# Kernel optimization log

Measured on AMD Instinct MI355X. Metric: run time of the kernel, lower is better.

## Reference

```python
import jax, jax.numpy as jnp
import numpy as np

N = 50000      # nodes
E = 800000     # edges (before self-loops)
F_IN = 128     # input node features
H = 5          # attention heads
C = 32         # per-head channels (hidden_channels // 5)
HC = H * C     # 160 = hidden_channels
G = 64         # graphs in batch


def setup_inputs() -> dict:
    key = jax.random.key(0)
    ks = jax.random.split(key, 20)
    p = lambda k, shape: jax.random.normal(k, shape, dtype=jnp.float32) * 0.1
    return {
        "x": jax.random.normal(ks[0], (N, F_IN), dtype=jnp.float32),
        "edge_index": jax.random.randint(ks[1], (2, E), 0, N),
        "edge_attr": jax.random.normal(ks[2], (E, 1), dtype=jnp.float32),
        "batch": jnp.sort(jax.random.randint(ks[3], (N,), 0, G)),
        # conv1 params (GATConv: lin, lin_edge, att_src, att_dst, att_edge, bias)
        "w1": p(ks[4], (F_IN, HC)), "we1": p(ks[5], (1, HC)),
        "as1": p(ks[6], (H, C)), "ad1": p(ks[7], (H, C)), "ae1": p(ks[8], (H, C)),
        "b1": jnp.zeros((HC,), jnp.float32),
        # conv2 params
        "w2": p(ks[9], (HC, HC)), "we2": p(ks[10], (1, HC)),
        "as2": p(ks[11], (H, C)), "ad2": p(ks[12], (H, C)), "ae2": p(ks[13], (H, C)),
        "b2": jnp.zeros((HC,), jnp.float32),
        # LayerNorms + merge MLP
        "ln1_g": jnp.ones((HC,), jnp.float32), "ln1_b": jnp.zeros((HC,), jnp.float32),
        "ln2_g": jnp.ones((HC,), jnp.float32), "ln2_b": jnp.zeros((HC,), jnp.float32),
        "mw": p(ks[14], (HC, HC)), "mb": jnp.zeros((HC,), jnp.float32),
    }


def _layernorm(x, g, b, eps=1e-5):
    m = x.mean(-1, keepdims=True)
    v = ((x - m) ** 2).mean(-1, keepdims=True)
    return (x - m) / jnp.sqrt(v + eps) * g + b


def _gat_layer(x, edge_index, edge_attr, w, we, a_s, a_d, a_e, b):
    """PyG GATConv with edge_dim, add_self_loops=True, fill_value='mean'."""
    src, dst = edge_index[0], edge_index[1]
    # self-loop edge_attr = mean of incoming edge attrs (scatter-mean onto dst)
    cnt = jax.ops.segment_sum(jnp.ones((E,), x.dtype), dst, num_segments=N)
    ea_mean = jax.ops.segment_sum(edge_attr, dst, num_segments=N) / jnp.maximum(cnt, 1.0)[:, None]
    loop = jnp.arange(N)
    src_f = jnp.concatenate([src, loop])
    dst_f = jnp.concatenate([dst, loop])
    ea_f = jnp.concatenate([edge_attr, ea_mean], axis=0)  # [E+N, 1]

    h = (x @ w).reshape(N, H, C)                           # [N,H,C]
    al_src = jnp.einsum('nhc,hc->nh', h, a_s)              # [N,H]
    al_dst = jnp.einsum('nhc,hc->nh', h, a_d)
    eh = (ea_f @ we).reshape(-1, H, C)                     # [E+N,H,C]
    al_e = jnp.einsum('ehc,hc->eh', eh, a_e)

    alpha = jax.nn.leaky_relu(al_src[src_f] + al_dst[dst_f] + al_e, 0.2)  # [E+N,H]
    amax = jax.ops.segment_max(alpha, dst_f, num_segments=N)
    ex = jnp.exp(alpha - amax[dst_f])
    den = jax.ops.segment_sum(ex, dst_f, num_segments=N)
    alpha = ex / den[dst_f]                                # segment softmax over dst

    out = jax.ops.segment_sum(h[src_f] * alpha[..., None], dst_f, num_segments=N)
    return out.reshape(N, HC) + b, alpha


def reference(x, edge_index, edge_attr, batch,
              w1, we1, as1, ad1, ae1, b1,
              w2, we2, as2, ad2, ae2, b2,
              ln1_g, ln1_b, ln2_g, ln2_b, mw, mb):
    x1, a1 = _gat_layer(x, edge_index, edge_attr, w1, we1, as1, ad1, ae1, b1)
    x1 = jax.nn.leaky_relu(x1, 0.01)
    x1 = _layernorm(x1, ln1_g, ln1_b)          # dropout = identity in eval
    x2, a2 = _gat_layer(x1, edge_index, edge_attr, w2, we2, as2, ad2, ae2, b2)
    x2 = jax.nn.leaky_relu(x2, 0.01)
    x2 = _layernorm(x2, ln2_g, ln2_b)
    x3 = jax.nn.leaky_relu(x2 @ mw + mb, 0.01)
    gcnt = jax.ops.segment_sum(jnp.ones((N,), x3.dtype), batch, num_segments=G)
    pooled = jax.ops.segment_sum(x3, batch, num_segments=G) / jnp.maximum(gcnt, 1.0)[:, None]
    return x3, pooled, a1, a2
```

## Files before the change

### kernel.cpp

```cpp
#include <hip/hip_runtime.h>
#include <hip/hip_fp16.h>
#include <math.h>

#define NN 50000
#define EE 800000
#define FIN 128
#define NH 5
#define HC 160
#define NG 64
#define CH2 32
#define NB 160
#define EPB 5000
#define NW 12500
#define ALS8 8
#define LOG2E 1.4426950408889634f
#define WPAD 168
#define IPAD 40

typedef _Float16 f16x8 __attribute__((ext_vector_type(8)));
typedef _Float16 f16x4 __attribute__((ext_vector_type(4)));
typedef float f32x4 __attribute__((ext_vector_type(4)));

__device__ __forceinline__ float lrelu(float x, float s) { return x >= 0.f ? x : s * x; }

__device__ __forceinline__ float4 h8_to_f4(uint2 u) {
    __half2 a = *reinterpret_cast<__half2*>(&u.x);
    __half2 b = *reinterpret_cast<__half2*>(&u.y);
    float2 fa = __half22float2(a), fb = __half22float2(b);
    return make_float4(fa.x, fa.y, fb.x, fb.y);
}

__global__ void prep_kernel(const int* __restrict__ batch, float* psum, int* gcnt,
                            const float* we1, const float* ae1,
                            const float* we2, const float* ae2, float* s_out,
                            int* dbin) {
    int i = blockIdx.x * 256 + threadIdx.x;
    if (i < NG * HC) psum[i] = 0.f;
    if (i < 256) dbin[i] = 0;
    if (i < NG) {
        int lo = 0, hi = NN;
        while (lo < hi) { int m = (lo + hi) >> 1; if (batch[m] < i) lo = m + 1; else hi = m; }
        int s = lo;
        lo = 0; hi = NN;
        int g1 = i + 1;
        while (lo < hi) { int m = (lo + hi) >> 1; if (batch[m] < g1) lo = m + 1; else hi = m; }
        gcnt[i] = lo - s;
    }
    if (i < 10) {
        const float* we = (i < 5) ? we1 : we2;
        const float* ae = (i < 5) ? ae1 : ae2;
        int h = i % 5;
        float s = 0.f;
        for (int c = 0; c < 32; c++) s += we[h * 32 + c] * ae[h * 32 + c];
        s_out[i] = s * LOG2E;
    }
}

__global__ void prepw_kernel(const float* __restrict__ w1, const float* __restrict__ w2,
                             const float* __restrict__ mw,
                             __half* wt1, __half* wt2, __half* wt3) {
    int i = blockIdx.x * 256 + threadIdx.x;
    if (i < 160 * 128) {
        int c = i >> 7, k = i & 127;
        wt1[i] = __float2half(w1[k * HC + c]);
    }
    if (i < 160 * 160) {
        int c = i / 160, k = i - c * 160;
        wt2[i] = __float2half(w2[k * HC + c]);
        wt3[i] = __float2half(mw[k * HC + c]);
    }
}

__global__ __launch_bounds__(256) void hist_kernel(const int* __restrict__ ei,
                                                   unsigned* __restrict__ hist_g) {
    __shared__ unsigned lh[NW];
    int b = blockIdx.x, tid = threadIdx.x;
    for (int w = tid; w < NW; w += 256) lh[w] = 0;
    __syncthreads();
    const int* dstp = ei + EE + b * EPB;
    for (int i = tid; i < EPB; i += 256) {
        int d = dstp[i];
        atomicAdd(&lh[d >> 2], 1u << ((d & 3) * 8));
    }
    __syncthreads();
    unsigned* outp = hist_g + (size_t)b * NW;
    for (int w = tid; w < NW; w += 256) outp[w] = lh[w];
}

__global__ void sscan_kernel(const unsigned* __restrict__ hist_g,
                             unsigned short* __restrict__ base_g, int* __restrict__ deg,
                             int* __restrict__ dbin) {
    __shared__ int lbin[256];
    int tid = threadIdx.x;
    int w = blockIdx.x * 256 + tid;
    lbin[tid] = 0;
    __syncthreads();
    if (w < NW) {
        unsigned r0 = 0, r1 = 0, r2 = 0, r3 = 0;
        for (int b = 0; b < NB; b++) {
            unsigned x = hist_g[(size_t)b * NW + w];
            uint2 st;
            st.x = r0 | (r1 << 16);
            st.y = r2 | (r3 << 16);
            *reinterpret_cast<uint2*>(&base_g[(size_t)b * NN + 4 * w]) = st;
            r0 += x & 0xffu; r1 += (x >> 8) & 0xffu; r2 += (x >> 16) & 0xffu; r3 += (x >> 24) & 0xffu;
        }
        uint4 dv; dv.x = r0; dv.y = r1; dv.z = r2; dv.w = r3;
        *reinterpret_cast<uint4*>(&deg[4 * w]) = dv;
        atomicAdd(&lbin[255 - (int)(r0 > 255u ? 255u : r0)], 1);
        atomicAdd(&lbin[255 - (int)(r1 > 255u ? 255u : r1)], 1);
        atomicAdd(&lbin[255 - (int)(r2 > 255u ? 255u : r2)], 1);
        atomicAdd(&lbin[255 - (int)(r3 > 255u ? 255u : r3)], 1);
    }
    __syncthreads();
    if (lbin[tid]) atomicAdd(&dbin[tid], lbin[tid]);
}

__global__ void scan1_kernel(const int* __restrict__ deg, int* bsum) {
    __shared__ int ws[4];
    int tid = threadIdx.x, lane = tid & 63, wid = tid >> 6;
    int i = blockIdx.x * 256 + tid;
    int v = (i < NN) ? deg[i] : 0;
    for (int o = 32; o >= 1; o >>= 1) v += __shfl_down(v, o, 64);
    if (lane == 0) ws[wid] = v;
    __syncthreads();
    if (tid == 0) bsum[blockIdx.x] = ws[0] + ws[1] + ws[2] + ws[3];
}

__global__ void scan2_kernel(int* bsum, int* boff, const int* __restrict__ dbin,
                             int* __restrict__ dpos) {
    __shared__ int ws[4];
    int tid = threadIdx.x, lane = tid & 63, wid = tid >> 6;
    int v = (tid < 196) ? bsum[tid] : 0;
    int x = v;
    for (int o = 1; o < 64; o <<= 1) {
        int t = __shfl_up(x, o, 64);
        if (lane >= o) x += t;
    }
    if (lane == 63) ws[wid] = x;
    __syncthreads();
    if (tid == 0) {
        int acc = 0;
        for (int w = 0; w < 4; w++) { int t = ws[w]; ws[w] = acc; acc += t; }
    }
    __syncthreads();
    if (tid < 196) boff[tid] = x + ws[wid] - v;
    __syncthreads();
    int bv = dbin[tid];
    int bx = bv;
    for (int o = 1; o < 64; o <<= 1) {
        int t = __shfl_up(bx, o, 64);
        if (lane >= o) bx += t;
    }
    if (lane == 63) ws[wid] = bx;
    __syncthreads();
    if (tid == 0) {
        int acc = 0;
        for (int w = 0; w < 4; w++) { int t = ws[w]; ws[w] = acc; acc += t; }
    }
    __syncthreads();
    dpos[tid] = bx + ws[wid] - bv;
}

__global__ void scan3_kernel(const int* __restrict__ deg, const int* __restrict__ boff,
                             int* off, int* __restrict__ dpos, int* __restrict__ perm) {
    __shared__ int ws[4];
    __shared__ int lbin[256];
    __shared__ int lbase[256];
    int tid = threadIdx.x, lane = tid & 63, wid = tid >> 6;
    int i = blockIdx.x * 256 + tid;
    int v = (i < NN) ? deg[i] : 0;
    lbin[tid] = 0;
    int x = v;
    for (int o = 1; o < 64; o <<= 1) {
        int t = __shfl_up(x, o, 64);
        if (lane >= o) x += t;
    }
    if (lane == 63) ws[wid] = x;
    __syncthreads();
    if (tid == 0) {
        int acc = 0;
        for (int w = 0; w < 4; w++) { int t = ws[w]; ws[w] = acc; acc += t; }
    }
    __syncthreads();
    int incl = x + ws[wid] + boff[blockIdx.x];
    int bin = 255 - (v > 255 ? 255 : v);
    int rank = 0;
    if (i < NN) {
        off[i + 1] = incl;
        rank = atomicAdd(&lbin[bin], 1);
    }
    if (i == 0) off[0] = 0;
    __syncthreads();
    if (lbin[tid] > 0) lbase[tid] = atomicAdd(&dpos[tid], lbin[tid]);
    __syncthreads();
    if (i < NN) perm[lbase[bin] + rank] = i;
}

__global__ __launch_bounds__(256) void scatter_kernel(const int* __restrict__ ei,
                                                      const float* __restrict__ ea,
                                                      const unsigned short* __restrict__ base_g,
                                                      const int* __restrict__ soff,
                                                      uint4* __restrict__ erec) {
    __shared__ unsigned lc[NW];
    int b = blockIdx.x, tid = threadIdx.x;
    for (int w = tid; w < NW; w += 256) lc[w] = 0;
    __syncthreads();
    int e0 = b * EPB;
    const unsigned short* brow = base_g + (size_t)b * NN;
    for (int i = tid; i < EPB; i += 256) {
        int e = e0 + i;
        int d = ei[EE + e];
        int sh = (d & 3) * 8;
        unsigned old = atomicAdd(&lc[d >> 2], 1u << sh);
        int r = (int)((old >> sh) & 0xffu);
        int pos = soff[d] + (int)brow[d] + r;
        uint4 rec;
        rec.x = (unsigned)ei[e];
        rec.y = (unsigned)e;
        rec.z = __float_as_uint(ea[e]);
        rec.w = 0;
        erec[pos] = rec;
    }
}

template <int K, typename AT>
__global__ __launch_bounds__(128, 4) void gemm_kernel(const AT* __restrict__ A,
                                                      const __half* __restrict__ Wt,
                                                      const float* __restrict__ a_s,
                                                      const float* __restrict__ a_d,
                                                      __half* __restrict__ out,
                                                      float* __restrict__ al_s,
                                                      float* __restrict__ al_d) {
    __shared__ __align__(16) char smem[16640];
    _Float16* Alds = (_Float16*)smem;
    _Float16* Bt   = (_Float16*)(smem + 2560);
    _Float16* Clds = (_Float16*)(smem + 2560);
    float* asld = (float*)(smem + 15360);
    float* adld = (float*)(smem + 16000);
    const int tid = threadIdx.x;
    const int w = tid >> 6, l = tid & 63;
    const int lr = l & 15, lq = l >> 4;
    const int base = blockIdx.x * 32;

    for (int i = tid; i < 160; i += 128) { asld[i] = a_s[i]; adld[i] = a_d[i]; }

    f32x4 acc[2][5];
#pragma unroll
    for (int mt = 0; mt < 2; mt++)
#pragma unroll
        for (int t = 0; t < 5; t++) acc[mt][t] = (f32x4){0.f, 0.f, 0.f, 0.f};

    for (int k0 = 0; k0 < K; k0 += 32) {
        __syncthreads();
        if constexpr (sizeof(AT) == 4) {
            for (int f = tid; f < 256; f += 128) {
                int row = f >> 3, q = f & 7;
                float4 av = make_float4(0.f, 0.f, 0.f, 0.f);
                if (base + row < NN)
                    av = *reinterpret_cast<const float4*>(&A[(size_t)(base + row) * K + k0 + q * 4]);
                f16x4 hv = {(_Float16)av.x, (_Float16)av.y, (_Float16)av.z, (_Float16)av.w};
                *reinterpret_cast<f16x4*>(&Alds[row * 40 + q * 4]) = hv;
            }
        } else {
            int row = tid >> 2, q = tid & 3;
            uint4 v = make_uint4(0, 0, 0, 0);
            if (base + row < NN)
                v = *reinterpret_cast<const uint4*>(&A[(size_t)(base + row) * K + k0 + q * 8]);
            *reinterpret_cast<uint4*>(&Alds[row * 40 + q * 8]) = v;
        }
        for (int f = tid; f < 640; f += 128) {
            int c = f >> 2, q = f & 3;
            uint4 v = *reinterpret_cast<const uint4*>(&Wt[(size_t)c * K + k0 + q * 8]);
            *reinterpret_cast<uint4*>(&Bt[c * 40 + q * 8]) = v;
        }
        __syncthreads();
        const f16x8 a0 = *reinterpret_cast<const f16x8*>(&Alds[lr * 40 + lq * 8]);
        const f16x8 a1 = *reinterpret_cast<const f16x8*>(&Alds[(16 + lr) * 40 + lq * 8]);
#pragma unroll
        for (int t = 0; t < 5; t++) {
            const f16x8 b = *reinterpret_cast<const f16x8*>(
                &Bt[((w * 5 + t) * 16 + lr) * 40 + lq * 8]);
            acc[0][t] = __builtin_amdgcn_mfma_f32_16x16x32_f16(a0, b, acc[0][t], 0, 0, 0);
            acc[1][t] = __builtin_amdgcn_mfma_f32_16x16x32_f16(a1, b, acc[1][t], 0, 0, 0);
        }
    }
    __syncthreads();
    _Float16* Cw = Clds + w * (32 * 88);
#pragma unroll
    for (int mt = 0; mt < 2; mt++)
#pragma unroll
        for (int t = 0; t < 5; t++)
#pragma unroll
            for (int j = 0; j < 4; j++)
                Cw[(mt * 16 + lq * 4 + j) * 88 + t * 16 + lr] = (_Float16)acc[mt][t][j];
    __syncthreads();
    for (int i = l; i < 320; i += 64) {
        int row = i / 10, q = i - row * 10;
        if (base + row < NN) {
            uint4 v = *reinterpret_cast<const uint4*>(&Cw[row * 88 + q * 8]);
            *reinterpret_cast<uint4*>(&out[(size_t)(base + row) * HC + w * 80 + q * 8]) = v;
        }
    }
    for (int f = tid; f < 320; f += 128) {
        int row = f / 10, rem = f - row * 10;
        int h = rem >> 1, sd = rem & 1;
        if (base + row < NN) {
            const float* av = (sd ? adld : asld) + h * 32;
            float s = 0.f;
#pragma unroll
            for (int c = 0; c < 32; c++) {
                int col = h * 32 + c;
                int wv = col >= 80;
                s += (float)Clds[wv * (32 * 88) + row * 88 + (col - 80 * wv)] * av[c];
            }
            s *= LOG2E;
            if (sd) al_d[(size_t)(base + row) * NH + h] = s;
            else    al_s[(size_t)(base + row) * ALS8 + h] = s;
        }
    }
}

__global__ __launch_bounds__(256, 8) void aggregate_kernel(
    const int* __restrict__ perm,
    const int* __restrict__ soff, const uint4* __restrict__ erec,
    const __half* __restrict__ hfeat, const float* __restrict__ als,
    const float* __restrict__ al_d, const float* __restrict__ s_e,
    const float* __restrict__ bias, const float* __restrict__ g_ln,
    const float* __restrict__ b_ln,
    float* __restrict__ alpha_out, __half* __restrict__ x_out) {
    const int tid = threadIdx.x;
    const int grp = tid >> 4;
    const int sl = tid & 15;
    const int n = perm[blockIdx.x * 16 + grp];
    __shared__ float w_sh_all[16][WPAD];
    __shared__ int ioff_all[16][IPAD];
    float* w_sh = w_sh_all[grp];
    int* ioff_sh = ioff_all[grp];

    const int s0 = soff[n];
    const int deg = soff[n + 1] - s0;
    const int items = deg + 1;

    float adr[NH], ser[NH];
#pragma unroll
    for (int h = 0; h < NH; h++) { adr[h] = al_d[n * NH + h]; ser[h] = s_e[h]; }

    const int cA = sl * 4, cB = 64 + sl * 4, cC = 128 + sl * 2;
    const int hA = sl >> 3, hB = 2 + (sl >> 3);
    float4 accA = make_float4(0.f, 0.f, 0.f, 0.f);
    float4 accB = make_float4(0.f, 0.f, 0.f, 0.f);
    float2 accC = make_float2(0.f, 0.f);

    if (items <= CH2) {
        float rw[2][NH];
        float lm[NH];
#pragma unroll
        for (int h = 0; h < NH; h++) lm[h] = -3.0e38f;
        float eas = 0.f;
        int myy[2];
#pragma unroll
        for (int t = 0; t < 2; t++) {
            if (deg > 16 * t) {
                int i = sl + 16 * t;
                if (i < deg) {
                    uint4 rec = erec[s0 + i];
                    int src = (int)rec.x;
                    float eav = __uint_as_float(rec.z);
                    ioff_sh[i] = src * (HC * 2);
                    myy[t] = (int)rec.y;
                    eas += eav;
                    const float* ap = als + (size_t)src * ALS8;
                    float4 a4 = *reinterpret_cast<const float4*>(ap);
                    float a5 = ap[4];
                    float asv[5] = {a4.x, a4.y, a4.z, a4.w, a5};
#pragma unroll
                    for (int h = 0; h < NH; h++) {
                        float r = lrelu(asv[h] + adr[h] + eav * ser[h], 0.2f);
                        rw[t][h] = r;
                        lm[h] = fmaxf(lm[h], r);
                    }
                }
            }
        }
#pragma unroll
        for (int o = 1; o < 16; o <<= 1) {
#pragma unroll
            for (int h = 0; h < NH; h++) lm[h] = fmaxf(lm[h], __shfl_xor(lm[h], o, 64));
            eas += __shfl_xor(eas, o, 64);
        }
        float emean = eas / fmaxf((float)deg, 1.f);
        float m[NH], rs[NH];
        {
            const float* ap = als + (size_t)n * ALS8;
            float4 a4 = *reinterpret_cast<const float4*>(ap);
            float a5 = ap[4];
            float asv[5] = {a4.x, a4.y, a4.z, a4.w, a5};
#pragma unroll
            for (int h = 0; h < NH; h++) {
                rs[h] = lrelu(asv[h] + adr[h] + emean * ser[h], 0.2f);
                m[h] = fmaxf(lm[h], rs[h]);
            }
        }
        float ls[NH] = {0.f, 0.f, 0.f, 0.f, 0.f};
#pragma unroll
        for (int t = 0; t < 2; t++) {
            if (items > 16 * t) {
                int i = sl + 16 * t;
                if (i < deg) {
#pragma unroll
                    for (int h = 0; h < NH; h++) {
                        float w = exp2f(rw[t][h] - m[h]);
                        rw[t][h] = w;
                        ls[h] += w;
                    }
                } else if (i == deg) {
                    ioff_sh[i] = n * (HC * 2);
#pragma unroll
                    for (int h = 0; h < NH; h++) {
                        float w = exp2f(rs[h] - m[h]);
                        rw[t][h] = w;
                        ls[h] += w;
                    }
                }
            }
        }
#pragma unroll
        for (int o = 1; o < 16; o <<= 1) {
#pragma unroll
            for (int h = 0; h < NH; h++) ls[h] += __shfl_xor(ls[h], o, 64);
        }
        float dinv[NH];
#pragma unroll
        for (int h = 0; h < NH; h++) dinv[h] = 1.f / ls[h];
#pragma unroll
        for (int t = 0; t < 2; t++) {
            if (items > 16 * t) {
                int i = sl + 16 * t;
                if (i < items) {
                    int opos = (i < deg) ? myy[t] : (EE + n);
#pragma unroll
                    for (int h = 0; h < NH; h++) {
                        float w = rw[t][h] * dinv[h];
                        w_sh[i * NH + h] = w;
                        alpha_out[(size_t)opos * NH + h] = w;
                    }
                }
            }
        }
        const char* hb = (const char*)hfeat;
        for (int i0 = 0; i0 < items; i0 += 4) {
            float wA[4], wB[4], wC[4];
            uint2 vA[4], vB[4];
            unsigned vC[4];
#pragma unroll
            for (int j = 0; j < 4; j++) {
                int i = i0 + j;
                bool ok = i < items;
                int ii = ok ? i : 0;
                const char* rp = hb + (size_t)(unsigned)ioff_sh[ii];
                wA[j] = ok ? w_sh[ii * NH + hA] : 0.f;
                wB[j] = ok ? w_sh[ii * NH + hB] : 0.f;
                wC[j] = ok ? w_sh[ii * NH + 4] : 0.f;
                vA[j] = *reinterpret_cast<const uint2*>(rp + cA * 2);
                vB[j] = *reinterpret_cast<const uint2*>(rp + cB * 2);
                vC[j] = *reinterpret_cast<const unsigned*>(rp + cC * 2);
            }
#pragma unroll
            for (int j = 0; j < 4; j++) {
                float4 fA = h8_to_f4(vA[j]);
                accA.x += wA[j] * fA.x; accA.y += wA[j] * fA.y;
                accA.z += wA[j] * fA.z; accA.w += wA[j] * fA.w;
                float4 fB = h8_to_f4(vB[j]);
                accB.x += wB[j] * fB.x; accB.y += wB[j] * fB.y;
                accB.z += wB[j] * fB.z; accB.w += wB[j] * fB.w;
                __half2 pC = *reinterpret_cast<__half2*>(&vC[j]);
                accC.x += wC[j] * __low2float(pC);
                accC.y += wC[j] * __high2float(pC);
            }
        }
    } else {
        float lm[NH];
#pragma unroll
        for (int h = 0; h < NH; h++) lm[h] = -3.0e38f;
        float eas = 0.f;
        for (int i = sl; i < deg; i += 16) {
            uint4 rec = erec[s0 + i];
            int src = (int)rec.x;
            float eav = __uint_as_float(rec.z);
            eas += eav;
            const float* ap = als + (size_t)src * ALS8;
            float4 a4 = *reinterpret_cast<const float4*>(ap);
            float a5 = ap[4];
            float asv[5] = {a4.x, a4.y, a4.z, a4.w, a5};
#pragma unroll
            for (int h = 0; h < NH; h++) {
                float r = lrelu(asv[h] + adr[h] + eav * ser[h], 0.2f);
                lm[h] = fmaxf(lm[h], r);
            }
        }
#pragma unroll
        for (int o = 1; o < 16; o <<= 1) {
#pragma unroll
            for (int h = 0; h < NH; h++) lm[h] = fmaxf(lm[h], __shfl_xor(lm[h], o, 64));
            eas += __shfl_xor(eas, o, 64);
        }
        float emean = eas / fmaxf((float)deg, 1.f);
        float m[NH], rs[NH];
        {
            const float* ap = als + (size_t)n * ALS8;
#pragma unroll
            for (int h = 0; h < NH; h++) {
                rs[h] = lrelu(ap[h] + adr[h] + emean * ser[h], 0.2f);
                m[h] = fmaxf(lm[h], rs[h]);
            }
        }
        float ls[NH] = {0.f, 0.f, 0.f, 0.f, 0.f};
        for (int i = sl; i < items; i += 16) {
            int src; float eav;
            if (i < deg) { uint4 rec = erec[s0 + i]; src = (int)rec.x; eav = __uint_as_float(rec.z); }
            else         { src = n; eav = emean; }
            const float* ap = als + (size_t)src * ALS8;
#pragma unroll
            for (int h = 0; h < NH; h++) {
                float r = lrelu(ap[h] + adr[h] + eav * ser[h], 0.2f);
                ls[h] += exp2f(r - m[h]);
            }
        }
#pragma unroll
        for (int o = 1; o < 16; o <<= 1) {
#pragma unroll
            for (int h = 0; h < NH; h++) ls[h] += __shfl_xor(ls[h], o, 64);
        }
        float dinv[NH];
#pragma unroll
        for (int h = 0; h < NH; h++) dinv[h] = 1.f / ls[h];
        for (int i = sl; i < items; i += 16) {
            int src; float eav; int opos;
            if (i < deg) { uint4 rec = erec[s0 + i]; src = (int)rec.x; eav = __uint_as_float(rec.z); opos = (int)rec.y; }
            else         { src = n; eav = emean; opos = EE + n; }
            const float* ap = als + (size_t)src * ALS8;
#pragma unroll
            for (int h = 0; h < NH; h++) {
                float r = lrelu(ap[h] + adr[h] + eav * ser[h], 0.2f);
                alpha_out[(size_t)opos * NH + h] = exp2f(r - m[h]) * dinv[h];
            }
        }
        for (int i = 0; i < items; i++) {
            int src; float eav;
            if (i < deg) { uint4 rec = erec[s0 + i]; src = (int)rec.x; eav = __uint_as_float(rec.z); }
            else         { src = n; eav = emean; }
            const float* ap = als + (size_t)src * ALS8;
            float wAv = exp2f(lrelu(ap[hA] + adr[hA] + eav * ser[hA], 0.2f) - m[hA]) * dinv[hA];
            float wBv = exp2f(lrelu(ap[hB] + adr[hB] + eav * ser[hB], 0.2f) - m[hB]) * dinv[hB];
            float wCv = exp2f(lrelu(ap[4] + adr[4] + eav * ser[4], 0.2f) - m[4]) * dinv[4];
            const char* rp = (const char*)hfeat + (size_t)src * (HC * 2);
            uint2 vA = *reinterpret_cast<const uint2*>(rp + cA * 2);
            uint2 vB = *reinterpret_cast<const uint2*>(rp + cB * 2);
            unsigned vC = *reinterpret_cast<const unsigned*>(rp + cC * 2);
            float4 fA = h8_to_f4(vA);
            accA.x += wAv * fA.x; accA.y += wAv * fA.y;
            accA.z += wAv * fA.z; accA.w += wAv * fA.w;
            float4 fB = h8_to_f4(vB);
            accB.x += wBv * fB.x; accB.y += wBv * fB.y;
            accB.z += wBv * fB.z; accB.w += wBv * fB.w;
            __half2 pC = *reinterpret_cast<__half2*>(&vC);
            accC.x += wCv * __low2float(pC);
            accC.y += wCv * __high2float(pC);
        }
    }

    const float4 bA = *reinterpret_cast<const float4*>(&bias[cA]);
    const float4 bB = *reinterpret_cast<const float4*>(&bias[cB]);
    const float2 bC = *reinterpret_cast<const float2*>(&bias[cC]);
    float v0 = lrelu(accA.x + bA.x, 0.01f);
    float v1 = lrelu(accA.y + bA.y, 0.01f);
    float v2 = lrelu(accA.z + bA.z, 0.01f);
    float v3 = lrelu(accA.w + bA.w, 0.01f);
    float v4 = lrelu(accB.x + bB.x, 0.01f);
    float v5 = lrelu(accB.y + bB.y, 0.01f);
    float v6 = lrelu(accB.z + bB.z, 0.01f);
    float v7 = lrelu(accB.w + bB.w, 0.01f);
    float v8 = lrelu(accC.x + bC.x, 0.01f);
    float v9 = lrelu(accC.y + bC.y, 0.01f);
    float p1 = v0 + v1 + v2 + v3 + v4 + v5 + v6 + v7 + v8 + v9;
    float p2 = v0 * v0 + v1 * v1 + v2 * v2 + v3 * v3 + v4 * v4 +
               v5 * v5 + v6 * v6 + v7 * v7 + v8 * v8 + v9 * v9;
#pragma unroll
    for (int o = 1; o < 16; o <<= 1) {
        p1 += __shfl_xor(p1, o, 64);
        p2 += __shfl_xor(p2, o, 64);
    }
    float mean = p1 * (1.f / (float)HC);
    float var = p2 * (1.f / (float)HC) - mean * mean;
    float rstd = rsqrtf(var + 1e-5f);
    const float4 gA = *reinterpret_cast<const float4*>(&g_ln[cA]);
    const float4 gB = *reinterpret_cast<const float4*>(&g_ln[cB]);
    const float2 gC = *reinterpret_cast<const float2*>(&g_ln[cC]);
    const float4 tA = *reinterpret_cast<const float4*>(&b_ln[cA]);
    const float4 tB = *reinterpret_cast<const float4*>(&b_ln[cB]);
    const float2 tC = *reinterpret_cast<const float2*>(&b_ln[cC]);
    float o0 = (v0 - mean) * rstd * gA.x + tA.x;
    float o1 = (v1 - mean) * rstd * gA.y + tA.y;
    float o2 = (v2 - mean) * rstd * gA.z + tA.z;
    float o3 = (v3 - mean) * rstd * gA.w + tA.w;
    float o4 = (v4 - mean) * rstd * gB.x + tB.x;
    float o5 = (v5 - mean) * rstd * gB.y + tB.y;
    float o6 = (v6 - mean) * rstd * gB.z + tB.z;
    float o7 = (v7 - mean) * rstd * gB.w + tB.w;
    float o8 = (v8 - mean) * rstd * gC.x + tC.x;
    float o9 = (v9 - mean) * rstd * gC.y + tC.y;
    {
        __half2 hA01 = __floats2half2_rn(o0, o1);
        __half2 hA23 = __floats2half2_rn(o2, o3);
        uint2 stA;
        stA.x = *reinterpret_cast<unsigned*>(&hA01);
        stA.y = *reinterpret_cast<unsigned*>(&hA23);
        *reinterpret_cast<uint2*>(&x_out[(size_t)n * HC + cA]) = stA;
        __half2 hB01 = __floats2half2_rn(o4, o5);
        __half2 hB23 = __floats2half2_rn(o6, o7);
        uint2 stB;
        stB.x = *reinterpret_cast<unsigned*>(&hB01);
        stB.y = *reinterpret_cast<unsigned*>(&hB23);
        *reinterpret_cast<uint2*>(&x_out[(size_t)n * HC + cB]) = stB;
        __half2 hC = __floats2half2_rn(o8, o9);
        *reinterpret_cast<unsigned*>(&x_out[(size_t)n * HC + cC]) =
            *reinterpret_cast<unsigned*>(&hC);
    }
}

__global__ __launch_bounds__(128, 4) void gemm3_kernel(const __half* __restrict__ A,
                                                       const __half* __restrict__ Wt,
                                                       const float* __restrict__ bias,
                                                       const int* __restrict__ batch,
                                                       float* __restrict__ x3,
                                                       float* __restrict__ psum) {
    __shared__ __align__(16) _Float16 Alds[32 * 40];
    __shared__ __align__(16) _Float16 Bt[160 * 40];
    __shared__ int bt[32];
    const int tid = threadIdx.x;
    const int w = tid >> 6, l = tid & 63;
    const int lr = l & 15, lq = l >> 4;
    const int base = blockIdx.x * 32;

    if (tid < 32) bt[tid] = batch[(base + tid < NN) ? (base + tid) : (NN - 1)];

    f32x4 acc[2][5];
#pragma unroll
    for (int mt = 0; mt < 2; mt++)
#pragma unroll
        for (int t = 0; t < 5; t++) acc[mt][t] = (f32x4){0.f, 0.f, 0.f, 0.f};

    for (int k0 = 0; k0 < HC; k0 += 32) {
        __syncthreads();
        {
            int row = tid >> 2, q = tid & 3;
            uint4 v = make_uint4(0, 0, 0, 0);
            if (base + row < NN)
                v = *reinterpret_cast<const uint4*>(&A[(size_t)(base + row) * HC + k0 + q * 8]);
            *reinterpret_cast<uint4*>(&Alds[row * 40 + q * 8]) = v;
        }
        for (int f = tid; f < 640; f += 128) {
            int c = f >> 2, q = f & 3;
            uint4 v = *reinterpret_cast<const uint4*>(&Wt[(size_t)c * HC + k0 + q * 8]);
            *reinterpret_cast<uint4*>(&Bt[c * 40 + q * 8]) = v;
        }
        __syncthreads();
        const f16x8 a0 = *reinterpret_cast<const f16x8*>(&Alds[lr * 40 + lq * 8]);
        const f16x8 a1 = *reinterpret_cast<const f16x8*>(&Alds[(16 + lr) * 40 + lq * 8]);
#pragma unroll
        for (int t = 0; t < 5; t++) {
            const f16x8 b = *reinterpret_cast<const f16x8*>(
                &Bt[((w * 5 + t) * 16 + lr) * 40 + lq * 8]);
            acc[0][t] = __builtin_amdgcn_mfma_f32_16x16x32_f16(a0, b, acc[0][t], 0, 0, 0);
            acc[1][t] = __builtin_amdgcn_mfma_f32_16x16x32_f16(a1, b, acc[1][t], 0, 0, 0);
        }
    }
#pragma unroll
    for (int t = 0; t < 5; t++) {
        int col = w * 80 + t * 16 + lr;
        float bj = bias[col];
        float run = 0.f;
        int g = bt[lq * 4];
#pragma unroll
        for (int mt = 0; mt < 2; mt++)
#pragma unroll
            for (int j = 0; j < 4; j++) {
                int row = mt * 16 + lq * 4 + j;
                bool ok = base + row < NN;
                float vv = lrelu(acc[mt][t][j] + bj, 0.01f);
                if (ok) x3[(size_t)(base + row) * HC + col] = vv;
                int gb = bt[row];
                if (gb != g) { atomicAdd(&psum[g * HC + col], run); run = 0.f; g = gb; }
                if (ok) run += vv;
            }
        atomicAdd(&psum[g * HC + col], run);
    }
}

__global__ void pooldiv_kernel(const float* __restrict__ psum, const int* __restrict__ gcnt,
                               float* pooled_out) {
    int i = blockIdx.x * 256 + threadIdx.x;
    if (i < NG * HC) pooled_out[i] = psum[i] / fmaxf((float)gcnt[i / HC], 1.f);
}

extern "C" void kernel_launch(void* const* d_in, const int* in_sizes, int n_in,
                              void* d_out, int out_size, void* d_ws, size_t ws_size,
                              hipStream_t stream) {
    const float* x    = (const float*)d_in[0];
    const int*   ei   = (const int*)d_in[1];
    const float* ea   = (const float*)d_in[2];
    const int*   batch= (const int*)d_in[3];
    const float* w1   = (const float*)d_in[4];
    const float* we1  = (const float*)d_in[5];
    const float* as1  = (const float*)d_in[6];
    const float* ad1  = (const float*)d_in[7];
    const float* ae1  = (const float*)d_in[8];
    const float* b1   = (const float*)d_in[9];
    const float* w2   = (const float*)d_in[10];
    const float* we2  = (const float*)d_in[11];
    const float* as2  = (const float*)d_in[12];
    const float* ad2  = (const float*)d_in[13];
    const float* ae2  = (const float*)d_in[14];
    const float* b2   = (const float*)d_in[15];
    const float* ln1g = (const float*)d_in[16];
    const float* ln1b = (const float*)d_in[17];
    const float* ln2g = (const float*)d_in[18];
    const float* ln2b = (const float*)d_in[19];
    const float* mw   = (const float*)d_in[20];
    const float* mb   = (const float*)d_in[21];

    float* out = (float*)d_out;
    float* pooled_out = out + (size_t)NN * HC;
    float* a1 = pooled_out + NG * HC;
    float* a2 = a1 + (size_t)(EE + NN) * NH;

    char* wp = (char*)d_ws;
    auto alloc = [&](size_t bytes) {
        void* p = (void*)wp;
        wp += (bytes + 255) & ~(size_t)255;
        return p;
    };
    char* region = (char*)alloc(32 * 1024 * 1024);
    __half* hbuf = (__half*)region;
    __half* x12h = (__half*)(region + 16 * 1024 * 1024);
    unsigned*       hist_g = (unsigned*)region;
    unsigned short* base_g = (unsigned short*)(region + 8 * 1024 * 1024);
    uint4* erec  = (uint4*)alloc((size_t)EE * 16);
    float* als   = (float*)alloc((size_t)NN * ALS8 * 4);
    float* ald   = (float*)alloc((size_t)NN * NH * 4);
    int*   deg   = (int*)alloc((size_t)NN * 4);
    int*   soff  = (int*)alloc((size_t)(NN + 1) * 4);
    float* sbuf  = (float*)alloc(64);
    float* psum  = (float*)alloc((size_t)NG * HC * 4);
    int*   gcnt  = (int*)alloc((size_t)NG * 4);
    int*   bsum  = (int*)alloc(256 * 4);
    int*   boff  = (int*)alloc(256 * 4);
    int*   dbin  = (int*)alloc(256 * 4);
    int*   dpos  = (int*)alloc(256 * 4);
    int*   perm  = (int*)alloc((size_t)NN * 4);
    __half* wt1  = (__half*)alloc((size_t)160 * 128 * 2);
    __half* wt2  = (__half*)alloc((size_t)160 * 160 * 2);
    __half* wt3  = (__half*)alloc((size_t)160 * 160 * 2);

    prep_kernel<<<40, 256, 0, stream>>>(batch, psum, gcnt, we1, ae1, we2, ae2, sbuf, dbin);
    prepw_kernel<<<100, 256, 0, stream>>>(w1, w2, mw, wt1, wt2, wt3);
    hist_kernel<<<NB, 256, 0, stream>>>(ei, hist_g);
    sscan_kernel<<<49, 256, 0, stream>>>(hist_g, base_g, deg, dbin);
    scan1_kernel<<<196, 256, 0, stream>>>(deg, bsum);
    scan2_kernel<<<1, 256, 0, stream>>>(bsum, boff, dbin, dpos);
    scan3_kernel<<<196, 256, 0, stream>>>(deg, boff, soff, dpos, perm);
    scatter_kernel<<<NB, 256, 0, stream>>>(ei, ea, base_g, soff, erec);

    const int GB = (NN + 31) / 32;

    gemm_kernel<128, float><<<GB, 128, 0, stream>>>(x, wt1, as1, ad1, hbuf, als, ald);
    aggregate_kernel<<<3125, 256, 0, stream>>>(perm, soff, erec, hbuf, als, ald,
                                               sbuf, b1, ln1g, ln1b, a1, x12h);

    gemm_kernel<160, __half><<<GB, 128, 0, stream>>>(x12h, wt2, as2, ad2, hbuf, als, ald);
    aggregate_kernel<<<3125, 256, 0, stream>>>(perm, soff, erec, hbuf, als, ald,
                                               sbuf + 5, b2, ln2g, ln2b, a2, x12h);

    gemm3_kernel<<<GB, 128, 0, stream>>>(x12h, wt3, mb, batch, out, psum);
    pooldiv_kernel<<<40, 256, 0, stream>>>(psum, gcnt, pooled_out);
}
```

Baseline: 438.7 us.

## Horizontally fuse prep, weight-prep and histogram kernels; run gemm1 alongside sscan

The three small setup kernels (prep, weight transpose/convert, destination histogram) become one launch, with each block range doing a different job. The segmented scan is merged with the first-layer GEMM in a single launch, so GEMM1 no longer waits for the scan and scatter chain. To allow this, the workspace is rearranged so hbuf no longer aliases the histogram and base buffers. The cost is that half the threads in each GEMM block exit immediately and the GEMM is compiled under different launch bounds, which may change its register allocation.

```diff
diff --git a/kernel.cpp b/kernel.cpp
--- a/kernel.cpp
+++ b/kernel.cpp
@@ -30,90 +30,194 @@
     return make_float4(fa.x, fa.y, fb.x, fb.y);
 }
 
-__global__ void prep_kernel(const int* __restrict__ batch, float* psum, int* gcnt,
-                            const float* we1, const float* ae1,
-                            const float* we2, const float* ae2, float* s_out,
-                            int* dbin) {
-    int i = blockIdx.x * 256 + threadIdx.x;
-    if (i < NG * HC) psum[i] = 0.f;
-    if (i < 256) dbin[i] = 0;
-    if (i < NG) {
-        int lo = 0, hi = NN;
-        while (lo < hi) { int m = (lo + hi) >> 1; if (batch[m] < i) lo = m + 1; else hi = m; }
-        int s = lo;
-        lo = 0; hi = NN;
-        int g1 = i + 1;
-        while (lo < hi) { int m = (lo + hi) >> 1; if (batch[m] < g1) lo = m + 1; else hi = m; }
-        gcnt[i] = lo - s;
-    }
-    if (i < 10) {
-        const float* we = (i < 5) ? we1 : we2;
-        const float* ae = (i < 5) ? ae1 : ae2;
-        int h = i % 5;
-        float s = 0.f;
-        for (int c = 0; c < 32; c++) s += we[h * 32 + c] * ae[h * 32 + c];
-        s_out[i] = s * LOG2E;
-    }
-}
-
-__global__ void prepw_kernel(const float* __restrict__ w1, const float* __restrict__ w2,
-                             const float* __restrict__ mw,
-                             __half* wt1, __half* wt2, __half* wt3) {
-    int i = blockIdx.x * 256 + threadIdx.x;
-    if (i < 160 * 128) {
-        int c = i >> 7, k = i & 127;
-        wt1[i] = __float2half(w1[k * HC + c]);
-    }
-    if (i < 160 * 160) {
-        int c = i / 160, k = i - c * 160;
-        wt2[i] = __float2half(w2[k * HC + c]);
-        wt3[i] = __float2half(mw[k * HC + c]);
-    }
-}
-
-__global__ __launch_bounds__(256) void hist_kernel(const int* __restrict__ ei,
-                                                   unsigned* __restrict__ hist_g) {
+__global__ __launch_bounds__(256) void prep_fused_kernel(
+    const int* __restrict__ batch, float* psum, int* gcnt,
+    const float* we1, const float* ae1, const float* we2, const float* ae2,
+    float* s_out, int* dbin,
+    const float* __restrict__ w1, const float* __restrict__ w2,
+    const float* __restrict__ mw, __half* wt1, __half* wt2, __half* wt3,
+    const int* __restrict__ ei, unsigned* __restrict__ hist_g) {
     __shared__ unsigned lh[NW];
-    int b = blockIdx.x, tid = threadIdx.x;
-    for (int w = tid; w < NW; w += 256) lh[w] = 0;
-    __syncthreads();
-    const int* dstp = ei + EE + b * EPB;
-    for (int i = tid; i < EPB; i += 256) {
-        int d = dstp[i];
-        atomicAdd(&lh[d >> 2], 1u << ((d & 3) * 8));
-    }
-    __syncthreads();
-    unsigned* outp = hist_g + (size_t)b * NW;
-    for (int w = tid; w < NW; w += 256) outp[w] = lh[w];
-}
-
-__global__ void sscan_kernel(const unsigned* __restrict__ hist_g,
-                             unsigned short* __restrict__ base_g, int* __restrict__ deg,
-                             int* __restrict__ dbin) {
-    __shared__ int lbin[256];
-    int tid = threadIdx.x;
-    int w = blockIdx.x * 256 + tid;
-    lbin[tid] = 0;
-    __syncthreads();
-    if (w < NW) {
-        unsigned r0 = 0, r1 = 0, r2 = 0, r3 = 0;
-        for (int b = 0; b < NB; b++) {
-            unsigned x = hist_g[(size_t)b * NW + w];
-            uint2 st;
-            st.x = r0 | (r1 << 16);
-            st.y = r2 | (r3 << 16);
-            *reinterpret_cast<uint2*>(&base_g[(size_t)b * NN + 4 * w]) = st;
-            r0 += x & 0xffu; r1 += (x >> 8) & 0xffu; r2 += (x >> 16) & 0xffu; r3 += (x >> 24) & 0xffu;
-        }
-        uint4 dv; dv.x = r0; dv.y = r1; dv.z = r2; dv.w = r3;
-        *reinterpret_cast<uint4*>(&deg[4 * w]) = dv;
-        atomicAdd(&lbin[255 - (int)(r0 > 255u ? 255u : r0)], 1);
-        atomicAdd(&lbin[255 - (int)(r1 > 255u ? 255u : r1)], 1);
-        atomicAdd(&lbin[255 - (int)(r2 > 255u ? 255u : r2)], 1);
-        atomicAdd(&lbin[255 - (int)(r3 > 255u ? 255u : r3)], 1);
-    }
-    __syncthreads();
-    if (lbin[tid]) atomicAdd(&dbin[tid], lbin[tid]);
+    const int b = blockIdx.x, tid = threadIdx.x;
+    if (b < 40) {
+        int i = b * 256 + tid;
+        if (i < NG * HC) psum[i] = 0.f;
+        if (i < 256) dbin[i] = 0;
+        if (i < NG) {
+            int lo = 0, hi = NN;
+            while (lo < hi) { int m = (lo + hi) >> 1; if (batch[m] < i) lo = m + 1; else hi = m; }
+            int s = lo;
+            lo = 0; hi = NN;
+            int g1 = i + 1;
+            while (lo < hi) { int m = (lo + hi) >> 1; if (batch[m] < g1) lo = m + 1; else hi = m; }
+            gcnt[i] = lo - s;
+        }
+        if (i < 10) {
+            const float* we = (i < 5) ? we1 : we2;
+            const float* ae = (i < 5) ? ae1 : ae2;
+            int h = i % 5;
+            float s = 0.f;
+            for (int c = 0; c < 32; c++) s += we[h * 32 + c] * ae[h * 32 + c];
+            s_out[i] = s * LOG2E;
+        }
+    } else if (b < 140) {
+        int i = (b - 40) * 256 + tid;
+        if (i < 160 * 128) {
+            int c = i >> 7, k = i & 127;
+            wt1[i] = __float2half(w1[k * HC + c]);
+        }
+        if (i < 160 * 160) {
+            int c = i / 160, k = i - c * 160;
+            wt2[i] = __float2half(w2[k * HC + c]);
+            wt3[i] = __float2half(mw[k * HC + c]);
+        }
+    } else {
+        int bb = b - 140;
+        for (int w = tid; w < NW; w += 256) lh[w] = 0;
+        __syncthreads();
+        const int* dstp = ei + EE + bb * EPB;
+        for (int i = tid; i < EPB; i += 256) {
+            int d = dstp[i];
+            atomicAdd(&lh[d >> 2], 1u << ((d & 3) * 8));
+        }
+        __syncthreads();
+        unsigned* outp = hist_g + (size_t)bb * NW;
+        for (int w = tid; w < NW; w += 256) outp[w] = lh[w];
+    }
+}
+
+template <int K, typename AT>
+__device__ __forceinline__ void gemm_body(int bidx, int tid, char* smem,
+                                          const AT* __restrict__ A,
+                                          const __half* __restrict__ Wt,
+                                          const float* __restrict__ a_s,
+                                          const float* __restrict__ a_d,
+                                          __half* __restrict__ out,
+                                          float* __restrict__ al_s,
+                                          float* __restrict__ al_d) {
+    _Float16* Alds = (_Float16*)smem;
+    _Float16* Bt   = (_Float16*)(smem + 2560);
+    _Float16* Clds = (_Float16*)(smem + 2560);
+    float* asld = (float*)(smem + 15360);
+    float* adld = (float*)(smem + 16000);
+    const int w = tid >> 6, l = tid & 63;
+    const int lr = l & 15, lq = l >> 4;
+    const int base = bidx * 32;
+
+    for (int i = tid; i < 160; i += 128) { asld[i] = a_s[i]; adld[i] = a_d[i]; }
+
+    f32x4 acc[2][5];
+#pragma unroll
+    for (int mt = 0; mt < 2; mt++)
+#pragma unroll
+        for (int t = 0; t < 5; t++) acc[mt][t] = (f32x4){0.f, 0.f, 0.f, 0.f};
+
+    for (int k0 = 0; k0 < K; k0 += 32) {
+        __syncthreads();
+        if constexpr (sizeof(AT) == 4) {
+            for (int f = tid; f < 256; f += 128) {
+                int row = f >> 3, q = f & 7;
+                float4 av = make_float4(0.f, 0.f, 0.f, 0.f);
+                if (base + row < NN)
+                    av = *reinterpret_cast<const float4*>(&A[(size_t)(base + row) * K + k0 + q * 4]);
+                f16x4 hv = {(_Float16)av.x, (_Float16)av.y, (_Float16)av.z, (_Float16)av.w};
+                *reinterpret_cast<f16x4*>(&Alds[row * 40 + q * 4]) = hv;
+            }
+        } else {
+            int row = tid >> 2, q = tid & 3;
+            uint4 v = make_uint4(0, 0, 0, 0);
+            if (base + row < NN)
+                v = *reinterpret_cast<const uint4*>(&A[(size_t)(base + row) * K + k0 + q * 8]);
+            *reinterpret_cast<uint4*>(&Alds[row * 40 + q * 8]) = v;
+        }
+        for (int f = tid; f < 640; f += 128) {
+            int c = f >> 2, q = f & 3;
+            uint4 v = *reinterpret_cast<const uint4*>(&Wt[(size_t)c * K + k0 + q * 8]);
+            *reinterpret_cast<uint4*>(&Bt[c * 40 + q * 8]) = v;
+        }
+        __syncthreads();
+        const f16x8 a0 = *reinterpret_cast<const f16x8*>(&Alds[lr * 40 + lq * 8]);
+        const f16x8 a1 = *reinterpret_cast<const f16x8*>(&Alds[(16 + lr) * 40 + lq * 8]);
+#pragma unroll
+        for (int t = 0; t < 5; t++) {
+            const f16x8 b = *reinterpret_cast<const f16x8*>(
+                &Bt[((w * 5 + t) * 16 + lr) * 40 + lq * 8]);
+            acc[0][t] = __builtin_amdgcn_mfma_f32_16x16x32_f16(a0, b, acc[0][t], 0, 0, 0);
+            acc[1][t] = __builtin_amdgcn_mfma_f32_16x16x32_f16(a1, b, acc[1][t], 0, 0, 0);
+        }
+    }
+    __syncthreads();
+    _Float16* Cw = Clds + w * (32 * 88);
+#pragma unroll
+    for (int mt = 0; mt < 2; mt++)
+#pragma unroll
+        for (int t = 0; t < 5; t++)
+#pragma unroll
+            for (int j = 0; j < 4; j++)
+                Cw[(mt * 16 + lq * 4 + j) * 88 + t * 16 + lr] = (_Float16)acc[mt][t][j];
+    __syncthreads();
+    for (int i = l; i < 320; i += 64) {
+        int row = i / 10, q = i - row * 10;
+        if (base + row < NN) {
+            uint4 v = *reinterpret_cast<const uint4*>(&Cw[row * 88 + q * 8]);
+            *reinterpret_cast<uint4*>(&out[(size_t)(base + row) * HC + w * 80 + q * 8]) = v;
+        }
+    }
+    for (int f = tid; f < 320; f += 128) {
+        int row = f / 10, rem = f - row * 10;
+        int h = rem >> 1, sd = rem & 1;
+        if (base + row < NN) {
+            const float* av = (sd ? adld : asld) + h * 32;
+            float s = 0.f;
+#pragma unroll
+            for (int c = 0; c < 32; c++) {
+                int col = h * 32 + c;
+                int wv = col >= 80;
+                s += (float)Clds[wv * (32 * 88) + row * 88 + (col - 80 * wv)] * av[c];
+            }
+            s *= LOG2E;
+            if (sd) al_d[(size_t)(base + row) * NH + h] = s;
+            else    al_s[(size_t)(base + row) * ALS8 + h] = s;
+        }
+    }
+}
+
+__global__ __launch_bounds__(256, 4) void sscan_gemm1_kernel(
+    const unsigned* __restrict__ hist_g, unsigned short* __restrict__ base_g,
+    int* __restrict__ deg, int* __restrict__ dbin,
+    const float* __restrict__ A, const __half* __restrict__ Wt,
+    const float* __restrict__ a_s, const float* __restrict__ a_d,
+    __half* __restrict__ out, float* __restrict__ al_s, float* __restrict__ al_d) {
+    __shared__ __align__(16) char smem[16640];
+    const int tid = threadIdx.x;
+    if (blockIdx.x < 49) {
+        int* lbin = (int*)smem;
+        int w = blockIdx.x * 256 + tid;
+        lbin[tid] = 0;
+        __syncthreads();
+        if (w < NW) {
+            unsigned r0 = 0, r1 = 0, r2 = 0, r3 = 0;
+            for (int b = 0; b < NB; b++) {
+                unsigned x = hist_g[(size_t)b * NW + w];
+                uint2 st;
+                st.x = r0 | (r1 << 16);
+                st.y = r2 | (r3 << 16);
+                *reinterpret_cast<uint2*>(&base_g[(size_t)b * NN + 4 * w]) = st;
+                r0 += x & 0xffu; r1 += (x >> 8) & 0xffu; r2 += (x >> 16) & 0xffu; r3 += (x >> 24) & 0xffu;
+            }
+            uint4 dv; dv.x = r0; dv.y = r1; dv.z = r2; dv.w = r3;
+            *reinterpret_cast<uint4*>(&deg[4 * w]) = dv;
+            atomicAdd(&lbin[255 - (int)(r0 > 255u ? 255u : r0)], 1);
+            atomicAdd(&lbin[255 - (int)(r1 > 255u ? 255u : r1)], 1);
+            atomicAdd(&lbin[255 - (int)(r2 > 255u ? 255u : r2)], 1);
+            atomicAdd(&lbin[255 - (int)(r3 > 255u ? 255u : r3)], 1);
+        }
+        __syncthreads();
+        if (lbin[tid]) atomicAdd(&dbin[tid], lbin[tid]);
+    } else {
+        if (tid >= 128) return;
+        gemm_body<128, float>(blockIdx.x - 49, tid, smem, A, Wt, a_s, a_d, out, al_s, al_d);
+    }
 }
 
 __global__ void scan1_kernel(const int* __restrict__ deg, int* bsum) {
@@ -233,92 +337,7 @@
                                                       float* __restrict__ al_s,
                                                       float* __restrict__ al_d) {
     __shared__ __align__(16) char smem[16640];
-    _Float16* Alds = (_Float16*)smem;
-    _Float16* Bt   = (_Float16*)(smem + 2560);
-    _Float16* Clds = (_Float16*)(smem + 2560);
-    float* asld = (float*)(smem + 15360);
-    float* adld = (float*)(smem + 16000);
-    const int tid = threadIdx.x;
-    const int w = tid >> 6, l = tid & 63;
-    const int lr = l & 15, lq = l >> 4;
-    const int base = blockIdx.x * 32;
-
-    for (int i = tid; i < 160; i += 128) { asld[i] = a_s[i]; adld[i] = a_d[i]; }
-
-    f32x4 acc[2][5];
-#pragma unroll
-    for (int mt = 0; mt < 2; mt++)
-#pragma unroll
-        for (int t = 0; t < 5; t++) acc[mt][t] = (f32x4){0.f, 0.f, 0.f, 0.f};
-
-    for (int k0 = 0; k0 < K; k0 += 32) {
-        __syncthreads();
-        if constexpr (sizeof(AT) == 4) {
-            for (int f = tid; f < 256; f += 128) {
-                int row = f >> 3, q = f & 7;
-                float4 av = make_float4(0.f, 0.f, 0.f, 0.f);
-                if (base + row < NN)
-                    av = *reinterpret_cast<const float4*>(&A[(size_t)(base + row) * K + k0 + q * 4]);
-                f16x4 hv = {(_Float16)av.x, (_Float16)av.y, (_Float16)av.z, (_Float16)av.w};
-                *reinterpret_cast<f16x4*>(&Alds[row * 40 + q * 4]) = hv;
-            }
-        } else {
-            int row = tid >> 2, q = tid & 3;
-            uint4 v = make_uint4(0, 0, 0, 0);
-            if (base + row < NN)
-                v = *reinterpret_cast<const uint4*>(&A[(size_t)(base + row) * K + k0 + q * 8]);
-            *reinterpret_cast<uint4*>(&Alds[row * 40 + q * 8]) = v;
-        }
-        for (int f = tid; f < 640; f += 128) {
-            int c = f >> 2, q = f & 3;
-            uint4 v = *reinterpret_cast<const uint4*>(&Wt[(size_t)c * K + k0 + q * 8]);
-            *reinterpret_cast<uint4*>(&Bt[c * 40 + q * 8]) = v;
-        }
-        __syncthreads();
-        const f16x8 a0 = *reinterpret_cast<const f16x8*>(&Alds[lr * 40 + lq * 8]);
-        const f16x8 a1 = *reinterpret_cast<const f16x8*>(&Alds[(16 + lr) * 40 + lq * 8]);
-#pragma unroll
-        for (int t = 0; t < 5; t++) {
-            const f16x8 b = *reinterpret_cast<const f16x8*>(
-                &Bt[((w * 5 + t) * 16 + lr) * 40 + lq * 8]);
-            acc[0][t] = __builtin_amdgcn_mfma_f32_16x16x32_f16(a0, b, acc[0][t], 0, 0, 0);
-            acc[1][t] = __builtin_amdgcn_mfma_f32_16x16x32_f16(a1, b, acc[1][t], 0, 0, 0);
-        }
-    }
-    __syncthreads();
-    _Float16* Cw = Clds + w * (32 * 88);
-#pragma unroll
-    for (int mt = 0; mt < 2; mt++)
-#pragma unroll
-        for (int t = 0; t < 5; t++)
-#pragma unroll
-            for (int j = 0; j < 4; j++)
-                Cw[(mt * 16 + lq * 4 + j) * 88 + t * 16 + lr] = (_Float16)acc[mt][t][j];
-    __syncthreads();
-    for (int i = l; i < 320; i += 64) {
-        int row = i / 10, q = i - row * 10;
-        if (base + row < NN) {
-            uint4 v = *reinterpret_cast<const uint4*>(&Cw[row * 88 + q * 8]);
-            *reinterpret_cast<uint4*>(&out[(size_t)(base + row) * HC + w * 80 + q * 8]) = v;
-        }
-    }
-    for (int f = tid; f < 320; f += 128) {
-        int row = f / 10, rem = f - row * 10;
-        int h = rem >> 1, sd = rem & 1;
-        if (base + row < NN) {
-            const float* av = (sd ? adld : asld) + h * 32;
-            float s = 0.f;
-#pragma unroll
-            for (int c = 0; c < 32; c++) {
-                int col = h * 32 + c;
-                int wv = col >= 80;
-                s += (float)Clds[wv * (32 * 88) + row * 88 + (col - 80 * wv)] * av[c];
-            }
-            s *= LOG2E;
-            if (sd) al_d[(size_t)(base + row) * NH + h] = s;
-            else    al_s[(size_t)(base + row) * ALS8 + h] = s;
-        }
-    }
+    gemm_body<K, AT>(blockIdx.x, threadIdx.x, smem, A, Wt, a_s, a_d, out, al_s, al_d);
 }
 
 __global__ __launch_bounds__(256, 8) void aggregate_kernel(
@@ -741,11 +760,11 @@
         wp += (bytes + 255) & ~(size_t)255;
         return p;
     };
-    char* region = (char*)alloc(32 * 1024 * 1024);
-    __half* hbuf = (__half*)region;
-    __half* x12h = (__half*)(region + 16 * 1024 * 1024);
+    char* region = (char*)alloc(40 * 1024 * 1024);
     unsigned*       hist_g = (unsigned*)region;
     unsigned short* base_g = (unsigned short*)(region + 8 * 1024 * 1024);
+    __half* hbuf = (__half*)(region + 24 * 1024 * 1024);
+    __half* x12h = (__half*)region;
     uint4* erec  = (uint4*)alloc((size_t)EE * 16);
     float* als   = (float*)alloc((size_t)NN * ALS8 * 4);
     float* ald   = (float*)alloc((size_t)NN * NH * 4);
@@ -763,18 +782,18 @@
     __half* wt2  = (__half*)alloc((size_t)160 * 160 * 2);
     __half* wt3  = (__half*)alloc((size_t)160 * 160 * 2);
 
-    prep_kernel<<<40, 256, 0, stream>>>(batch, psum, gcnt, we1, ae1, we2, ae2, sbuf, dbin);
-    prepw_kernel<<<100, 256, 0, stream>>>(w1, w2, mw, wt1, wt2, wt3);
-    hist_kernel<<<NB, 256, 0, stream>>>(ei, hist_g);
-    sscan_kernel<<<49, 256, 0, stream>>>(hist_g, base_g, deg, dbin);
+    const int GB = (NN + 31) / 32;
+
+    prep_fused_kernel<<<300, 256, 0, stream>>>(batch, psum, gcnt, we1, ae1, we2, ae2,
+                                               sbuf, dbin, w1, w2, mw, wt1, wt2, wt3,
+                                               ei, hist_g);
+    sscan_gemm1_kernel<<<49 + GB, 256, 0, stream>>>(hist_g, base_g, deg, dbin,
+                                                    x, wt1, as1, ad1, hbuf, als, ald);
     scan1_kernel<<<196, 256, 0, stream>>>(deg, bsum);
     scan2_kernel<<<1, 256, 0, stream>>>(bsum, boff, dbin, dpos);
     scan3_kernel<<<196, 256, 0, stream>>>(deg, boff, soff, dpos, perm);
     scatter_kernel<<<NB, 256, 0, stream>>>(ei, ea, base_g, soff, erec);
 
-    const int GB = (NN + 31) / 32;
-
-    gemm_kernel<128, float><<<GB, 128, 0, stream>>>(x, wt1, as1, ad1, hbuf, als, ald);
     aggregate_kernel<<<3125, 256, 0, stream>>>(perm, soff, erec, hbuf, als, ald,
                                                sbuf, b1, ln1g, ln1b, a1, x12h);
 
```

Result: faster. 415.4 us (-5.3%).
